# Kernel optimization log

Measured on AMD Instinct MI355X. Metric: run time of the kernel, lower is better.

The kernel has to match this reference:

```python
import jax, jax.numpy as jnp
import numpy as np

N_NODES = 100000
N_EDGES = 1600000
F_IN = 32
HID = 64


def _gcn_conv(x, edge_index, edge_weight, W, b):
    """PyG GCNConv with edge_weight: add self-loops, symmetric degree norm, scatter-add."""
    N = x.shape[0]
    xw = x @ W  # [N, out]
    row, col = edge_index[0], edge_index[1]
    loop = jnp.arange(N)
    row = jnp.concatenate([row, loop])
    col = jnp.concatenate([col, loop])
    ew = jnp.concatenate([edge_weight, jnp.ones((N,), dtype=x.dtype)])
    # degree on target nodes
    deg = jax.ops.segment_sum(ew, col, num_segments=N)
    dinv = jnp.where(deg > 0, jax.lax.rsqrt(deg), 0.0)
    norm = dinv[row] * ew * dinv[col]  # [E+N]
    msg = norm[:, None] * xw[row]      # gather + scale over edges
    out = jax.ops.segment_sum(msg, col, num_segments=N)  # scatter-add
    return out + b


def setup_inputs() -> dict:
    key = jax.random.key(0)
    k = jax.random.split(key, 8)
    x = jax.random.normal(k[0], (N_NODES, F_IN), dtype=jnp.float32)
    edge_index = jax.random.randint(k[1], (2, N_EDGES), 0, N_NODES, dtype=jnp.int64)
    edge_attr = jax.random.uniform(k[2], (N_EDGES, 1), dtype=jnp.float32)
    s1 = 1.0 / np.sqrt(F_IN)
    s2 = 1.0 / np.sqrt(HID)
    W1 = jax.random.normal(k[3], (F_IN, HID), dtype=jnp.float32) * s1
    b1 = jnp.zeros((HID,), dtype=jnp.float32)
    W2 = jax.random.normal(k[4], (HID, F_IN), dtype=jnp.float32) * s2
    b2 = jnp.zeros((F_IN,), dtype=jnp.float32)
    return {"x": x, "edge_index": edge_index, "edge_attr": edge_attr,
            "W1": W1, "b1": b1, "W2": W2, "b2": b2}


def reference(x, edge_index, edge_attr, W1, b1, W2, b2):
    ew = edge_attr.squeeze(-1)
    h = jax.nn.relu(_gcn_conv(x, edge_index, ew, W1, b1))
    out = jax.nn.relu(_gcn_conv(h, edge_index, ew, W2, b2))
    return (out, edge_attr)
```

## Files before the change

### kernel.cpp

```cpp
#include <hip/hip_runtime.h>

#define NN 100000
#define NE 1600000
#define FIN 32
#define FHID 64

#define CLB 8
#define BN (1 << CLB)
#define NB ((NN + BN - 1) / BN)
#define NDB 128
#define CHUNK ((NE + NDB - 1) / NDB)
#define NSC (NB * NDB)
#define SCAN_B 1024
#define SCAN_NB ((NSC + SCAN_B - 1) / SCAN_B)
#define RCAP 12

#define LGKM0 asm volatile("s_waitcnt lgkmcnt(0)" ::: "memory")

__device__ __forceinline__ float lo16(unsigned g) {
    return __uint_as_float(g << 16);
}
__device__ __forceinline__ float hi16(unsigned g) {
    return __uint_as_float(g & 0xFFFF0000u);
}
__device__ __forceinline__ unsigned pack_bf16(float a, float b) {
    unsigned ua = __float_as_uint(a);
    unsigned ub = __float_as_uint(b);
    ua += 0x7FFFu + ((ua >> 16) & 1u);
    ub += 0x7FFFu + ((ub >> 16) & 1u);
    return (ua >> 16) | (ub & 0xFFFF0000u);
}

__global__ __launch_bounds__(512) void k_dcount(const int* __restrict__ col,
                                                int* __restrict__ hist_g) {
    __shared__ int hc[NB];
    for (int i = threadIdx.x; i < NB; i += blockDim.x) hc[i] = 0;
    __syncthreads();
    int beg = blockIdx.x * CHUNK, end = min(beg + CHUNK, NE);
    for (int e = beg + threadIdx.x; e < end; e += blockDim.x)
        atomicAdd(&hc[col[e] >> CLB], 1);
    __syncthreads();
    for (int i = threadIdx.x; i < NB; i += blockDim.x)
        hist_g[i * NDB + blockIdx.x] = hc[i];
}

__global__ void k_scan1(const int* __restrict__ in, int* __restrict__ out,
                        int* __restrict__ bsum) {
    __shared__ int s[SCAN_B];
    int i = blockIdx.x * SCAN_B + threadIdx.x;
    int v = (i < NSC) ? in[i] : 0;
    s[threadIdx.x] = v;
    __syncthreads();
    for (int o = 1; o < SCAN_B; o <<= 1) {
        int t = (threadIdx.x >= o) ? s[threadIdx.x - o] : 0;
        __syncthreads();
        s[threadIdx.x] += t;
        __syncthreads();
    }
    if (i < NSC) out[i] = s[threadIdx.x] - v;
    if (threadIdx.x == SCAN_B - 1) bsum[blockIdx.x] = s[SCAN_B - 1];
}

__global__ void k_scan2(int* __restrict__ bsum) {
    __shared__ int s[256];
    int v = (threadIdx.x < SCAN_NB) ? bsum[threadIdx.x] : 0;
    s[threadIdx.x] = v;
    __syncthreads();
    for (int o = 1; o < 256; o <<= 1) {
        int t = (threadIdx.x >= o) ? s[threadIdx.x - o] : 0;
        __syncthreads();
        s[threadIdx.x] += t;
        __syncthreads();
    }
    if (threadIdx.x < SCAN_NB) bsum[threadIdx.x] = s[threadIdx.x] - v;
}

__global__ void k_scan3(int* __restrict__ out, const int* __restrict__ bsum) {
    int i = blockIdx.x * blockDim.x + threadIdx.x;
    if (i < NSC) out[i] += bsum[i >> 10];
}

__global__ __launch_bounds__(512) void k_dwrite(
        const int* __restrict__ row, const int* __restrict__ col,
        const float* __restrict__ ew, const int* __restrict__ base_g,
        uint2* __restrict__ rec0) {
    __shared__ int rk[NB];
    __shared__ int bl[NB];
    for (int i = threadIdx.x; i < NB; i += blockDim.x) {
        rk[i] = 0;
        bl[i] = base_g[i * NDB + blockIdx.x];
    }
    __syncthreads();
    int beg = blockIdx.x * CHUNK, end = min(beg + CHUNK, NE);
    for (int e = beg + threadIdx.x; e < end; e += blockDim.x) {
        int c = col[e];
        int bk = c >> CLB;
        int r = atomicAdd(&rk[bk], 1);
        unsigned pack = ((unsigned)(c & (BN - 1)) << 17) | (unsigned)row[e];
        rec0[bl[bk] + r] = make_uint2(pack, __float_as_uint(ew[e]));
    }
}

__global__ __launch_bounds__(512) void k_bsort(
        const int* __restrict__ base_g, const uint2* __restrict__ rec0,
        uint2* __restrict__ csr, int* __restrict__ rowptr,
        float* __restrict__ dinv) {
    __shared__ int cnt[BN];
    __shared__ int bas[BN];
    __shared__ int cur[BN];
    __shared__ float dg[BN];
    int tid = threadIdx.x;
    int b = blockIdx.x;
    int beg = base_g[b * NDB];
    int end = (b == NB - 1) ? NE : base_g[(b + 1) * NDB];
    if (tid < BN) { cnt[tid] = 0; dg[tid] = 0.0f; }
    __syncthreads();
    uint2 rc[RCAP];
#pragma unroll
    for (int i = 0; i < RCAP; ++i) {
        int j = beg + tid + i * 512;
        if (j < end) {
            uint2 p = rec0[j];
            rc[i] = p;
            atomicAdd(&cnt[p.x >> 17], 1);
            atomicAdd(&dg[p.x >> 17], __uint_as_float(p.y));
        } else {
            rc[i] = make_uint2(0u, 0u);
        }
    }
    __syncthreads();
    int v0 = (tid < BN) ? cnt[tid] : 0;
    __syncthreads();
    for (int o = 1; o < BN; o <<= 1) {
        int t = (tid < BN && tid >= o) ? cnt[tid - o] : 0;
        __syncthreads();
        if (tid < BN) cnt[tid] += t;
        __syncthreads();
    }
    if (tid < BN) {
        int excl = cnt[tid] - v0;
        bas[tid] = excl;
        cur[tid] = 0;
        int node = b * BN + tid;
        if (node < NN) {
            rowptr[node] = beg + excl;
            dinv[node] = rsqrtf(1.0f + dg[tid]);
        }
    }
    if (b == 0 && tid == 0) rowptr[NN] = NE;
    __syncthreads();
#pragma unroll
    for (int i = 0; i < RCAP; ++i) {
        int j = beg + tid + i * 512;
        if (j < end) {
            uint2 p = rc[i];
            int cl = p.x >> 17;
            int r = atomicAdd(&cur[cl], 1);
            csr[beg + bas[cl] + r] = make_uint2(p.x & 0x1FFFFu, p.y);
        }
    }
}

__global__ void k_scalex(const float* __restrict__ x, const float* __restrict__ dinv,
                         unsigned* __restrict__ xp) {
    int idx = blockIdx.x * blockDim.x + threadIdx.x;
    if (idx >= NN * (FIN / 2)) return;
    float dn = dinv[idx >> 4];
    float2 v = ((const float2*)x)[idx];
    xp[idx] = pack_bf16(v.x * dn, v.y * dn);
}

__global__ __launch_bounds__(256) void k_agg1p(
        const int* __restrict__ rowptr, const uint2* __restrict__ csr,
        const uint2* __restrict__ xp2, const float* __restrict__ dinv,
        uint2* __restrict__ pre) {
    int wid = (blockIdx.x * blockDim.x + threadIdx.x) >> 6;
    int lane = threadIdx.x & 63;
    int n = wid * 2 + (lane >> 5);
    if (n >= NN) return;
    int s = (lane & 31) >> 3;
    int u = lane & 7;
    int beg = rowptr[n], end = rowptr[n + 1];
    float dn = dinv[n];
    uint2 gs = xp2[(size_t)n * 8 + u];
    float c0 = 0.f, c1 = 0.f, c2 = 0.f, c3 = 0.f;
    float d0 = 0.f, d1 = 0.f, d2 = 0.f, d3 = 0.f;
    int j = beg + s;
    for (; j + 4 < end; j += 8) {
        uint2 e0 = csr[j];
        uint2 e1 = csr[j + 4];
        uint2 g0 = xp2[(size_t)e0.x * 8 + u];
        uint2 g1 = xp2[(size_t)e1.x * 8 + u];
        float w0 = __uint_as_float(e0.y);
        float w1 = __uint_as_float(e1.y);
        c0 = fmaf(w0, lo16(g0.x), c0);
        c1 = fmaf(w0, hi16(g0.x), c1);
        c2 = fmaf(w0, lo16(g0.y), c2);
        c3 = fmaf(w0, hi16(g0.y), c3);
        d0 = fmaf(w1, lo16(g1.x), d0);
        d1 = fmaf(w1, hi16(g1.x), d1);
        d2 = fmaf(w1, lo16(g1.y), d2);
        d3 = fmaf(w1, hi16(g1.y), d3);
    }
    for (; j < end; j += 4) {
        uint2 e = csr[j];
        uint2 g = xp2[(size_t)e.x * 8 + u];
        float w = __uint_as_float(e.y);
        c0 = fmaf(w, lo16(g.x), c0);
        c1 = fmaf(w, hi16(g.x), c1);
        c2 = fmaf(w, lo16(g.y), c2);
        c3 = fmaf(w, hi16(g.y), c3);
    }
    c0 += d0; c1 += d1; c2 += d2; c3 += d3;
#pragma unroll
    for (int m = 8; m <= 16; m <<= 1) {
        c0 += __shfl_xor(c0, m, 64);
        c1 += __shfl_xor(c1, m, 64);
        c2 += __shfl_xor(c2, m, 64);
        c3 += __shfl_xor(c3, m, 64);
    }
    if (s == 0) {
        float p0 = dn * (c0 + lo16(gs.x));
        float p1 = dn * (c1 + hi16(gs.x));
        float p2 = dn * (c2 + lo16(gs.y));
        float p3 = dn * (c3 + hi16(gs.y));
        pre[(size_t)n * 8 + u] = make_uint2(pack_bf16(p0, p1), pack_bf16(p2, p3));
    }
}

__global__ __launch_bounds__(256) void k_mlp(
        const uint2* __restrict__ pre2, const float* __restrict__ dinv,
        const float* __restrict__ W1, const float* __restrict__ b1,
        const float* __restrict__ W2, unsigned* __restrict__ hw2p, int nwaves) {
    __shared__ float pre_lds[4 * FIN];
    __shared__ float hv_lds[4 * FHID];
    int lane = threadIdx.x & 63;
    int ws = threadIdx.x >> 6;
    int hh = lane >> 5;
    int f = lane & 31;
    int t = lane & 15;
    int o = lane;
    float W1col[FIN];
#pragma unroll
    for (int k = 0; k < FIN; ++k) W1col[k] = W1[k * FHID + o];
    float b1o = b1[o];
    float W2h[FIN];
#pragma unroll
    for (int k = 0; k < FIN; ++k) W2h[k] = W2[(hh * 32 + k) * FIN + f];

    int gw = (blockIdx.x * blockDim.x + threadIdx.x) >> 6;
    for (int n = gw; n < NN; n += nwaves) {
        float dn = dinv[n];
        if (lane < 8) {
            uint2 g = pre2[(size_t)n * 8 + lane];
            float4 pq = make_float4(lo16(g.x), hi16(g.x), lo16(g.y), hi16(g.y));
            *(float4*)&pre_lds[ws * FIN + 4 * lane] = pq;
        }
        LGKM0;
        float hacc = b1o;
#pragma unroll
        for (int i = 0; i < 8; ++i) {
            float4 qd = *(const float4*)&pre_lds[ws * FIN + 4 * i];
            hacc = fmaf(qd.x, W1col[4 * i + 0], hacc);
            hacc = fmaf(qd.y, W1col[4 * i + 1], hacc);
            hacc = fmaf(qd.z, W1col[4 * i + 2], hacc);
            hacc = fmaf(qd.w, W1col[4 * i + 3], hacc);
        }
        hacc = hacc > 0.0f ? hacc : 0.0f;
        hv_lds[ws * FHID + o] = hacc;
        LGKM0;
        float part = 0.0f;
#pragma unroll
        for (int i = 0; i < 8; ++i) {
            float4 qd = *(const float4*)&hv_lds[ws * FHID + hh * 32 + 4 * i];
            part = fmaf(qd.x, W2h[4 * i + 0], part);
            part = fmaf(qd.y, W2h[4 * i + 1], part);
            part = fmaf(qd.z, W2h[4 * i + 2], part);
            part = fmaf(qd.w, W2h[4 * i + 3], part);
        }
        part += __shfl_xor(part, 32, 64);
        float v = dn * part;
        float vlo = __shfl(v, 2 * t, 64);
        float vhi = __shfl(v, 2 * t + 1, 64);
        if (lane < 16) hw2p[(size_t)n * 16 + lane] = pack_bf16(vlo, vhi);
    }
}

__global__ __launch_bounds__(256) void k_agg2p(
        const int* __restrict__ rowptr, const uint2* __restrict__ csr,
        const uint2* __restrict__ hw2p2, const float* __restrict__ dinv,
        const float* __restrict__ b2, float* __restrict__ out) {
    int wid = (blockIdx.x * blockDim.x + threadIdx.x) >> 6;
    int lane = threadIdx.x & 63;
    int n = wid * 2 + (lane >> 5);
    if (n >= NN) return;
    int s = (lane & 31) >> 3;
    int u = lane & 7;
    int beg = rowptr[n], end = rowptr[n + 1];
    float dn = dinv[n];
    uint2 gs = hw2p2[(size_t)n * 8 + u];
    float c0 = 0.f, c1 = 0.f, c2 = 0.f, c3 = 0.f;
    float d0 = 0.f, d1 = 0.f, d2 = 0.f, d3 = 0.f;
    int j = beg + s;
    for (; j + 4 < end; j += 8) {
        uint2 e0 = csr[j];
        uint2 e1 = csr[j + 4];
        uint2 g0 = hw2p2[(size_t)e0.x * 8 + u];
        uint2 g1 = hw2p2[(size_t)e1.x * 8 + u];
        float w0 = __uint_as_float(e0.y);
        float w1 = __uint_as_float(e1.y);
        c0 = fmaf(w0, lo16(g0.x), c0);
        c1 = fmaf(w0, hi16(g0.x), c1);
        c2 = fmaf(w0, lo16(g0.y), c2);
        c3 = fmaf(w0, hi16(g0.y), c3);
        d0 = fmaf(w1, lo16(g1.x), d0);
        d1 = fmaf(w1, hi16(g1.x), d1);
        d2 = fmaf(w1, lo16(g1.y), d2);
        d3 = fmaf(w1, hi16(g1.y), d3);
    }
    for (; j < end; j += 4) {
        uint2 e = csr[j];
        uint2 g = hw2p2[(size_t)e.x * 8 + u];
        float w = __uint_as_float(e.y);
        c0 = fmaf(w, lo16(g.x), c0);
        c1 = fmaf(w, hi16(g.x), c1);
        c2 = fmaf(w, lo16(g.y), c2);
        c3 = fmaf(w, hi16(g.y), c3);
    }
    c0 += d0; c1 += d1; c2 += d2; c3 += d3;
#pragma unroll
    for (int m = 8; m <= 16; m <<= 1) {
        c0 += __shfl_xor(c0, m, 64);
        c1 += __shfl_xor(c1, m, 64);
        c2 += __shfl_xor(c2, m, 64);
        c3 += __shfl_xor(c3, m, 64);
    }
    if (s == 0) {
        float4 bq = ((const float4*)b2)[u];
        float4 v;
        v.x = dn * (c0 + lo16(gs.x)) + bq.x;
        v.y = dn * (c1 + hi16(gs.x)) + bq.y;
        v.z = dn * (c2 + lo16(gs.y)) + bq.z;
        v.w = dn * (c3 + hi16(gs.y)) + bq.w;
        v.x = v.x > 0.f ? v.x : 0.f;
        v.y = v.y > 0.f ? v.y : 0.f;
        v.z = v.z > 0.f ? v.z : 0.f;
        v.w = v.w > 0.f ? v.w : 0.f;
        ((float4*)out)[(size_t)n * 8 + u] = v;
    }
}

extern "C" void kernel_launch(void* const* d_in, const int* in_sizes, int n_in,
                              void* d_out, int out_size, void* d_ws, size_t ws_size,
                              hipStream_t stream) {
    const float* x  = (const float*)d_in[0];
    const int*   ei = (const int*)d_in[1];
    const float* ea = (const float*)d_in[2];
    const float* W1 = (const float*)d_in[3];
    const float* b1 = (const float*)d_in[4];
    const float* W2 = (const float*)d_in[5];
    const float* b2 = (const float*)d_in[6];
    float* out = (float*)d_out;

    const int* row = ei;
    const int* col = ei + NE;

    char* w = (char*)d_ws;
    uint2* rec0     = (uint2*)w;
    uint2* csr      = rec0 + NE;
    unsigned* xp    = (unsigned*)(csr + NE);
    unsigned* hw2p  = xp + (size_t)NN * 16;
    unsigned* pre   = hw2p + (size_t)NN * 16;
    float* dinv     = (float*)(pre + (size_t)NN * 16);
    int*   rowptr   = (int*)(dinv + NN);
    int*   hist_g   = rowptr + NN + 1;
    int*   scng     = hist_g + NSC;
    int*   bsum     = scng + NSC;

    auto cdiv = [](long long a, int b) { return (int)((a + b - 1) / b); };
    const int PAIR_BLOCKS = cdiv((long long)cdiv(NN, 2) * 64, 256);

    hipMemcpyAsync(out + (size_t)NN * FIN, ea, sizeof(float) * (size_t)NE,
                   hipMemcpyDeviceToDevice, stream);

    k_dcount<<<NDB, 512, 0, stream>>>(col, hist_g);
    k_scan1<<<SCAN_NB, SCAN_B, 0, stream>>>(hist_g, scng, bsum);
    k_scan2<<<1, 256, 0, stream>>>(bsum);
    k_scan3<<<cdiv(NSC, 256), 256, 0, stream>>>(scng, bsum);
    k_dwrite<<<NDB, 512, 0, stream>>>(row, col, ea, scng, rec0);
    k_bsort<<<NB, 512, 0, stream>>>(scng, rec0, csr, rowptr, dinv);

    k_scalex<<<cdiv((long long)NN * (FIN / 2), 256), 256, 0, stream>>>(x, dinv, xp);

    k_agg1p<<<PAIR_BLOCKS, 256, 0, stream>>>(rowptr, csr, (const uint2*)xp, dinv,
                                             (uint2*)pre);
    const int MLP_BLOCKS = 2048;
    k_mlp<<<MLP_BLOCKS, 256, 0, stream>>>((const uint2*)pre, dinv, W1, b1, W2,
                                          hw2p, MLP_BLOCKS * 4);

    k_agg2p<<<PAIR_BLOCKS, 256, 0, stream>>>(rowptr, csr, (const uint2*)hw2p,
                                             dinv, b2, out);
}
```

Before: 159.2 us.

## Fuse edge-attr copy, scan fixup and x scaling into existing kernels; unroll gathers

The edge-attribute passthrough copy moves into the degree-count kernel, so the separate device-to-device memcpy goes away. The third scan pass is removed by adding the block offsets where the bases are read in k_dwrite and k_bsort. The x scale-and-pack-to-bf16 step now runs at the end of k_bsort using the per-block dinv held in shared memory. The aggregation loops are unrolled from 2 to 4 gathers per iteration for more memory-level parallelism. Together these drop three launches but add register pressure and a serial tail to k_bsort.

```diff
diff --git a/kernel.cpp b/kernel.cpp
--- a/kernel.cpp
+++ b/kernel.cpp
@@ -32,13 +32,17 @@
 }
 
 __global__ __launch_bounds__(512) void k_dcount(const int* __restrict__ col,
-                                                int* __restrict__ hist_g) {
+                                                const float* __restrict__ ea,
+                                                int* __restrict__ hist_g,
+                                                float* __restrict__ out_ea) {
     __shared__ int hc[NB];
     for (int i = threadIdx.x; i < NB; i += blockDim.x) hc[i] = 0;
     __syncthreads();
     int beg = blockIdx.x * CHUNK, end = min(beg + CHUNK, NE);
-    for (int e = beg + threadIdx.x; e < end; e += blockDim.x)
+    for (int e = beg + threadIdx.x; e < end; e += blockDim.x) {
         atomicAdd(&hc[col[e] >> CLB], 1);
+        out_ea[e] = ea[e];
+    }
     __syncthreads();
     for (int i = threadIdx.x; i < NB; i += blockDim.x)
         hist_g[i * NDB + blockIdx.x] = hc[i];
@@ -62,33 +66,29 @@
 }
 
 __global__ void k_scan2(int* __restrict__ bsum) {
-    __shared__ int s[256];
+    __shared__ int s[64];
     int v = (threadIdx.x < SCAN_NB) ? bsum[threadIdx.x] : 0;
     s[threadIdx.x] = v;
     __syncthreads();
-    for (int o = 1; o < 256; o <<= 1) {
+    for (int o = 1; o < 64; o <<= 1) {
         int t = (threadIdx.x >= o) ? s[threadIdx.x - o] : 0;
         __syncthreads();
         s[threadIdx.x] += t;
         __syncthreads();
     }
     if (threadIdx.x < SCAN_NB) bsum[threadIdx.x] = s[threadIdx.x] - v;
-}
-
-__global__ void k_scan3(int* __restrict__ out, const int* __restrict__ bsum) {
-    int i = blockIdx.x * blockDim.x + threadIdx.x;
-    if (i < NSC) out[i] += bsum[i >> 10];
 }
 
 __global__ __launch_bounds__(512) void k_dwrite(
         const int* __restrict__ row, const int* __restrict__ col,
         const float* __restrict__ ew, const int* __restrict__ base_g,
-        uint2* __restrict__ rec0) {
+        const int* __restrict__ bsum, uint2* __restrict__ rec0) {
     __shared__ int rk[NB];
     __shared__ int bl[NB];
     for (int i = threadIdx.x; i < NB; i += blockDim.x) {
         rk[i] = 0;
-        bl[i] = base_g[i * NDB + blockIdx.x];
+        int gi = i * NDB + blockIdx.x;
+        bl[i] = base_g[gi] + bsum[gi >> 10];
     }
     __syncthreads();
     int beg = blockIdx.x * CHUNK, end = min(beg + CHUNK, NE);
@@ -102,17 +102,21 @@
 }
 
 __global__ __launch_bounds__(512) void k_bsort(
-        const int* __restrict__ base_g, const uint2* __restrict__ rec0,
+        const int* __restrict__ base_g, const int* __restrict__ bsum,
+        const uint2* __restrict__ rec0, const float* __restrict__ x,
         uint2* __restrict__ csr, int* __restrict__ rowptr,
-        float* __restrict__ dinv) {
+        float* __restrict__ dinv, unsigned* __restrict__ xp) {
     __shared__ int cnt[BN];
     __shared__ int bas[BN];
     __shared__ int cur[BN];
     __shared__ float dg[BN];
+    __shared__ float dl[BN];
     int tid = threadIdx.x;
     int b = blockIdx.x;
-    int beg = base_g[b * NDB];
-    int end = (b == NB - 1) ? NE : base_g[(b + 1) * NDB];
+    int gi0 = b * NDB;
+    int beg = base_g[gi0] + bsum[gi0 >> 10];
+    int gi1 = (b + 1) * NDB;
+    int end = (b == NB - 1) ? NE : base_g[gi1] + bsum[gi1 >> 10];
     if (tid < BN) { cnt[tid] = 0; dg[tid] = 0.0f; }
     __syncthreads();
     uint2 rc[RCAP];
@@ -141,10 +145,12 @@
         int excl = cnt[tid] - v0;
         bas[tid] = excl;
         cur[tid] = 0;
+        float dn = rsqrtf(1.0f + dg[tid]);
+        dl[tid] = dn;
         int node = b * BN + tid;
         if (node < NN) {
             rowptr[node] = beg + excl;
-            dinv[node] = rsqrtf(1.0f + dg[tid]);
+            dinv[node] = dn;
         }
     }
     if (b == 0 && tid == 0) rowptr[NN] = NE;
@@ -159,15 +165,14 @@
             csr[beg + bas[cl] + r] = make_uint2(p.x & 0x1FFFFu, p.y);
         }
     }
-}
-
-__global__ void k_scalex(const float* __restrict__ x, const float* __restrict__ dinv,
-                         unsigned* __restrict__ xp) {
-    int idx = blockIdx.x * blockDim.x + threadIdx.x;
-    if (idx >= NN * (FIN / 2)) return;
-    float dn = dinv[idx >> 4];
-    float2 v = ((const float2*)x)[idx];
-    xp[idx] = pack_bf16(v.x * dn, v.y * dn);
+    for (int idx = tid; idx < BN * (FIN / 2); idx += 512) {
+        int nl = idx >> 4;
+        int node = b * BN + nl;
+        if (node >= NN) break;
+        float dn = dl[nl];
+        float2 v = ((const float2*)x)[(size_t)node * 16 + (idx & 15)];
+        xp[(size_t)node * 16 + (idx & 15)] = pack_bf16(v.x * dn, v.y * dn);
+    }
 }
 
 __global__ __launch_bounds__(256) void k_agg1p(
@@ -186,13 +191,19 @@
     float c0 = 0.f, c1 = 0.f, c2 = 0.f, c3 = 0.f;
     float d0 = 0.f, d1 = 0.f, d2 = 0.f, d3 = 0.f;
     int j = beg + s;
-    for (; j + 4 < end; j += 8) {
+    for (; j + 12 < end; j += 16) {
         uint2 e0 = csr[j];
         uint2 e1 = csr[j + 4];
+        uint2 e2 = csr[j + 8];
+        uint2 e3 = csr[j + 12];
         uint2 g0 = xp2[(size_t)e0.x * 8 + u];
         uint2 g1 = xp2[(size_t)e1.x * 8 + u];
+        uint2 g2 = xp2[(size_t)e2.x * 8 + u];
+        uint2 g3 = xp2[(size_t)e3.x * 8 + u];
         float w0 = __uint_as_float(e0.y);
         float w1 = __uint_as_float(e1.y);
+        float w2 = __uint_as_float(e2.y);
+        float w3 = __uint_as_float(e3.y);
         c0 = fmaf(w0, lo16(g0.x), c0);
         c1 = fmaf(w0, hi16(g0.x), c1);
         c2 = fmaf(w0, lo16(g0.y), c2);
@@ -201,6 +212,14 @@
         d1 = fmaf(w1, hi16(g1.x), d1);
         d2 = fmaf(w1, lo16(g1.y), d2);
         d3 = fmaf(w1, hi16(g1.y), d3);
+        c0 = fmaf(w2, lo16(g2.x), c0);
+        c1 = fmaf(w2, hi16(g2.x), c1);
+        c2 = fmaf(w2, lo16(g2.y), c2);
+        c3 = fmaf(w2, hi16(g2.y), c3);
+        d0 = fmaf(w3, lo16(g3.x), d0);
+        d1 = fmaf(w3, hi16(g3.x), d1);
+        d2 = fmaf(w3, lo16(g3.y), d2);
+        d3 = fmaf(w3, hi16(g3.y), d3);
     }
     for (; j < end; j += 4) {
         uint2 e = csr[j];
@@ -302,13 +321,19 @@
     float c0 = 0.f, c1 = 0.f, c2 = 0.f, c3 = 0.f;
     float d0 = 0.f, d1 = 0.f, d2 = 0.f, d3 = 0.f;
     int j = beg + s;
-    for (; j + 4 < end; j += 8) {
+    for (; j + 12 < end; j += 16) {
         uint2 e0 = csr[j];
         uint2 e1 = csr[j + 4];
+        uint2 e2 = csr[j + 8];
+        uint2 e3 = csr[j + 12];
         uint2 g0 = hw2p2[(size_t)e0.x * 8 + u];
         uint2 g1 = hw2p2[(size_t)e1.x * 8 + u];
+        uint2 g2 = hw2p2[(size_t)e2.x * 8 + u];
+        uint2 g3 = hw2p2[(size_t)e3.x * 8 + u];
         float w0 = __uint_as_float(e0.y);
         float w1 = __uint_as_float(e1.y);
+        float w2 = __uint_as_float(e2.y);
+        float w3 = __uint_as_float(e3.y);
         c0 = fmaf(w0, lo16(g0.x), c0);
         c1 = fmaf(w0, hi16(g0.x), c1);
         c2 = fmaf(w0, lo16(g0.y), c2);
@@ -317,6 +342,14 @@
         d1 = fmaf(w1, hi16(g1.x), d1);
         d2 = fmaf(w1, lo16(g1.y), d2);
         d3 = fmaf(w1, hi16(g1.y), d3);
+        c0 = fmaf(w2, lo16(g2.x), c0);
+        c1 = fmaf(w2, hi16(g2.x), c1);
+        c2 = fmaf(w2, lo16(g2.y), c2);
+        c3 = fmaf(w2, hi16(g2.y), c3);
+        d0 = fmaf(w3, lo16(g3.x), d0);
+        d1 = fmaf(w3, hi16(g3.x), d1);
+        d2 = fmaf(w3, lo16(g3.y), d2);
+        d3 = fmaf(w3, hi16(g3.y), d3);
     }
     for (; j < end; j += 4) {
         uint2 e = csr[j];
@@ -380,17 +413,11 @@
     auto cdiv = [](long long a, int b) { return (int)((a + b - 1) / b); };
     const int PAIR_BLOCKS = cdiv((long long)cdiv(NN, 2) * 64, 256);
 
-    hipMemcpyAsync(out + (size_t)NN * FIN, ea, sizeof(float) * (size_t)NE,
-                   hipMemcpyDeviceToDevice, stream);
-
-    k_dcount<<<NDB, 512, 0, stream>>>(col, hist_g);
+    k_dcount<<<NDB, 512, 0, stream>>>(col, ea, hist_g, out + (size_t)NN * FIN);
     k_scan1<<<SCAN_NB, SCAN_B, 0, stream>>>(hist_g, scng, bsum);
-    k_scan2<<<1, 256, 0, stream>>>(bsum);
-    k_scan3<<<cdiv(NSC, 256), 256, 0, stream>>>(scng, bsum);
-    k_dwrite<<<NDB, 512, 0, stream>>>(row, col, ea, scng, rec0);
-    k_bsort<<<NB, 512, 0, stream>>>(scng, rec0, csr, rowptr, dinv);
-
-    k_scalex<<<cdiv((long long)NN * (FIN / 2), 256), 256, 0, stream>>>(x, dinv, xp);
+    k_scan2<<<1, 64, 0, stream>>>(bsum);
+    k_dwrite<<<NDB, 512, 0, stream>>>(row, col, ea, scng, bsum, rec0);
+    k_bsort<<<NB, 512, 0, stream>>>(scng, bsum, rec0, x, csr, rowptr, dinv, xp);
 
     k_agg1p<<<PAIR_BLOCKS, 256, 0, stream>>>(rowptr, csr, (const uint2*)xp, dinv,
                                              (uint2*)pre);
```

After: 159.9 us. No clear change (+0.4%).
